# Performance work log

Measured on AMD Instinct MI355X. Metric: run time of the kernel, lower is better.

## Reference

```python
import jax, jax.numpy as jnp
import numpy as np

D_MODEL = 1024
N_HEADS = 16
HEAD_DIM = D_MODEL // N_HEADS


def setup_inputs() -> dict:
    key = jax.random.key(0)
    k_x, k_qkv, k_proj = jax.random.split(key, 3)
    x = jax.random.normal(k_x, (2, 2048, D_MODEL), dtype=jnp.float32)
    # flax nnx.Linear kernels: shape (in_features, out_features), lecun_normal-ish scale
    w_qkv = jax.random.normal(k_qkv, (D_MODEL, 3 * D_MODEL), dtype=jnp.float32) / np.sqrt(D_MODEL)
    w_proj = jax.random.normal(k_proj, (D_MODEL, D_MODEL), dtype=jnp.float32) / np.sqrt(D_MODEL)
    return {"x": x, "w_qkv": w_qkv, "w_proj": w_proj}


def reference(x, w_qkv, w_proj):
    bsz, seq_len, d_model = x.shape
    qkv = x @ w_qkv  # (B, T, 3*D)
    q, k, v = jnp.split(qkv, 3, axis=-1)
    q = q.reshape(bsz, seq_len, N_HEADS, HEAD_DIM)
    k = k.reshape(bsz, seq_len, N_HEADS, HEAD_DIM)
    v = v.reshape(bsz, seq_len, N_HEADS, HEAD_DIM)
    scale = jnp.sqrt(jnp.asarray(HEAD_DIM, dtype=x.dtype))
    attn_logits = jnp.einsum('bthd,bshd->bhts', q / scale, k)  # (B, H, T, T)
    attn_weights = jax.nn.softmax(attn_logits, axis=-1)
    attn_out = jnp.einsum('bhts,bshd->bthd', attn_weights, v)
    attn_out = attn_out.reshape(bsz, seq_len, d_model)
    return attn_out @ w_proj
```

## Files before the change

### kernel.cpp

```cpp
#include <hip/hip_runtime.h>
#include <hip/hip_bf16.h>
#include <cmath>

#define D_MODEL 1024
#define NH 16
#define HD 64
#define BSZ 2
#define SEQ 2048
#define MTOT (BSZ * SEQ)

typedef _Float16 f16x8 __attribute__((ext_vector_type(8)));
typedef __fp16   fp16x2 __attribute__((ext_vector_type(2)));
typedef float    f32x4  __attribute__((ext_vector_type(4)));
typedef float    f32x16 __attribute__((ext_vector_type(16)));
typedef unsigned int uivec2 __attribute__((ext_vector_type(2)));

#define QSCALE 0.18033688011112042f

__device__ __forceinline__ ushort f2h(float x) {
    union { _Float16 h; ushort u; } cv;
    cv.h = (_Float16)x;
    return cv.u;
}
__device__ __forceinline__ uint pkh(float a, float b) {
    union { fp16x2 h; uint u; } cv;
    cv.h = __builtin_amdgcn_cvt_pkrtz(a, b);
    return cv.u;
}
__device__ __forceinline__ float fexp2(float x) {
    float r; asm("v_exp_f32 %0, %1" : "=v"(r) : "v"(x)); return r;
}
__device__ __forceinline__ float fmax3(float a, float b, float c) {
    return fmaxf(fmaxf(a, b), c);
}
__device__ __forceinline__ void gload_lds16(const ushort* g, ushort* l) {
    __builtin_amdgcn_global_load_lds(
        (const __attribute__((address_space(1))) void*)g,
        (__attribute__((address_space(3))) void*)l, 16, 0, 0);
}

__global__ __launch_bounds__(256)
void cast8(const float* __restrict__ in, ushort* __restrict__ out, int n)
{
    const int i = (blockIdx.x * 256 + threadIdx.x) * 8;
    if (i >= n) return;
    float4 a = *(const float4*)(in + i);
    float4 b = *(const float4*)(in + i + 4);
    alignas(16) ushort h8[8];
    h8[0] = f2h(a.x); h8[1] = f2h(a.y); h8[2] = f2h(a.z); h8[3] = f2h(a.w);
    h8[4] = f2h(b.x); h8[5] = f2h(b.y); h8[6] = f2h(b.z); h8[7] = f2h(b.w);
    *(uint4*)(out + i) = *(const uint4*)h8;
}

__global__ __launch_bounds__(256)
void transpose_cast2(const float* __restrict__ A, const float* __restrict__ B,
                     ushort* __restrict__ At, ushort* __restrict__ Bt)
{
    __shared__ float tile[32][33];
    const int z = blockIdx.z;
    const float* in = (z < 3) ? A : B;
    ushort* out     = (z < 3) ? At : Bt;
    const int C     = (z < 3) ? 3 * D_MODEL : D_MODEL;
    const int cb    = (z < 3) ? z * 32 + blockIdx.x : blockIdx.x;
    const int R = D_MODEL;
    const int t  = threadIdx.x;
    const int r0 = blockIdx.y * 32, c0 = cb * 32;
    const int tr = t >> 5, tc = t & 31;
#pragma unroll
    for (int s = 0; s < 4; ++s)
        tile[tr + 8 * s][tc] = in[(size_t)(r0 + tr + 8 * s) * C + c0 + tc];
    __syncthreads();
#pragma unroll
    for (int s = 0; s < 4; ++s)
        out[(size_t)(c0 + tr + 8 * s) * R + r0 + tc] = f2h(tile[tc][tr + 8 * s]);
}

template <int MODE>
__global__ __launch_bounds__(256)
void gemm_mfma(const ushort* __restrict__ A, const ushort* __restrict__ Bt,
               float* __restrict__ outp,
               ushort* __restrict__ Qw, ushort* __restrict__ Kw,
               ushort* __restrict__ Vw, int N)
{
    __shared__ ushort As[2][128 * 32];
    __shared__ ushort Bs[2][128 * 32];

    const int t  = threadIdx.x;
    const int w  = t >> 6;
    const int l  = t & 63;
    const int lr = l & 15;
    const int lg = l >> 4;
    const int wr = w >> 1, wc = w & 1;
    const int m0 = blockIdx.y * 128, n0 = blockIdx.x * 128;

    const ushort* Ab = A  + (size_t)m0 * 1024;
    const ushort* Bb = Bt + (size_t)n0 * 1024;

    f32x4 acc[4][4];
#pragma unroll
    for (int i = 0; i < 4; ++i)
#pragma unroll
        for (int j = 0; j < 4; ++j) acc[i][j] = (f32x4){0.f, 0.f, 0.f, 0.f};

    auto stage = [&](int buf, int k0) {
#pragma unroll
        for (int s = 0; s < 2; ++s) {
            const int c    = s * 64 + l;
            const int row  = w * 32 + (c >> 2);
            const int unit = c & 3;
            gload_lds16(Ab + (size_t)row * 1024 + k0 + unit * 8,
                        &As[buf][(w * 128 + s * 64) * 8]);
            gload_lds16(Bb + (size_t)row * 1024 + k0 + unit * 8,
                        &Bs[buf][(w * 128 + s * 64) * 8]);
        }
    };

    stage(0, 0);
    __syncthreads();

    int cur = 0;
#pragma unroll 4
    for (int kt = 0; kt < 32; ++kt) {
        if (kt + 1 < 32) stage(cur ^ 1, (kt + 1) * 32);

        f16x8 af[4], bf[4];
#pragma unroll
        for (int m = 0; m < 4; ++m)
            af[m] = *(const f16x8*)&As[cur][(wr * 64 + m * 16 + lr) * 32 + lg * 8];
#pragma unroll
        for (int n = 0; n < 4; ++n)
            bf[n] = *(const f16x8*)&Bs[cur][(wc * 64 + n * 16 + lr) * 32 + lg * 8];
#pragma unroll
        for (int m = 0; m < 4; ++m)
#pragma unroll
            for (int n = 0; n < 4; ++n)
                acc[m][n] = __builtin_amdgcn_mfma_f32_16x16x32_f16(
                    af[m], bf[n], acc[m][n], 0, 0, 0);

        __syncthreads();
        cur ^= 1;
    }

    if (MODE == 1) {
#pragma unroll
        for (int mf = 0; mf < 4; ++mf) {
            const int row = m0 + wr * 64 + mf * 16 + lg * 4;
#pragma unroll
            for (int nf = 0; nf < 4; ++nf) {
                const int col = n0 + wc * 64 + nf * 16 + lr;
#pragma unroll
                for (int i = 0; i < 4; ++i)
                    outp[(size_t)(row + i) * N + col] = acc[mf][nf][i];
            }
        }
    } else {
#pragma unroll
        for (int mf = 0; mf < 4; ++mf) {
            const int row = m0 + wr * 64 + mf * 16 + lg * 4;
            const int b   = row >> 11;
            const int tt0 = row & (SEQ - 1);
#pragma unroll
            for (int nf = 0; nf < 4; ++nf) {
                const int col   = n0 + wc * 64 + nf * 16 + lr;
                const int which = col >> 10;
                const int h     = (col >> 6) & 15;
                const int d     = col & 63;
                if (which == 2) {
                    ushort* p = Vw + (((size_t)(b * NH + h) * HD + d) * SEQ) + tt0;
                    alignas(8) ushort e4[4];
#pragma unroll
                    for (int i = 0; i < 4; ++i) e4[i] = f2h(acc[mf][nf][i]);
                    *(uint2*)p = *(const uint2*)e4;
                } else {
                    ushort* dst = (which == 0) ? Qw : Kw;
                    const float sc = (which == 0) ? QSCALE : 1.0f;
#pragma unroll
                    for (int i = 0; i < 4; ++i)
                        dst[((size_t)(b * NH + h) * SEQ + tt0 + i) * HD + d] =
                            f2h(acc[mf][nf][i] * sc);
                }
            }
        }
    }
}

__global__ __launch_bounds__(512, 4)
void attn_mfma7(const ushort* __restrict__ Qw, const ushort* __restrict__ Kw,
                const ushort* __restrict__ Vtg, ushort* __restrict__ AO)
{
    __shared__ ushort KsAll[2][2][64 * 64];
    __shared__ ushort VtAll[2][2][64 * 64];

    const int t    = threadIdx.x;
    const int w    = t >> 6;
    const int l    = t & 63;
    const int q    = l & 31;
    const int hi   = l >> 5;
    const int half = w >> 2;
    const int ww   = w & 3;

    const int bh = blockIdx.y;
    const int q0 = blockIdx.x * 128 + ww * 32;
    const int kbase = half * (SEQ / 2);
    const int NT = (SEQ / 2) / 64;

    const ushort* Qp = Qw  + (size_t)bh * SEQ * HD;
    const ushort* Kp = Kw  + (size_t)bh * SEQ * HD;
    const ushort* Vp = Vtg + (size_t)bh * HD * SEQ;

    ushort (*Ks)[64 * 64] = KsAll[half];
    ushort (*Vt)[64 * 64] = VtAll[half];

    f16x8 qf[4];
#pragma unroll
    for (int kc = 0; kc < 4; ++kc)
        qf[kc] = *(const f16x8*)(Qp + (size_t)(q0 + q) * HD + kc * 16 + hi * 8);

    f32x16 oacc[2];
#pragma unroll
    for (int db = 0; db < 2; ++db)
#pragma unroll
        for (int r = 0; r < 16; ++r) oacc[db][r] = 0.f;
    float m_run = -3.0e38f, l_run = 0.f;

    auto stageK = [&](int buf, int k0) {
#pragma unroll
        for (int s = 0; s < 2; ++s) {
            const int c    = ww * 64 + l + 256 * s;
            const int row  = c >> 3;
            const int unit = (c & 7) ^ (row & 7);
            gload_lds16(Kp + (size_t)(k0 + row) * HD + unit * 8,
                        &Ks[buf][(ww * 64 + 256 * s) * 8]);
        }
    };
    auto stageV = [&](int buf, int k0) {
#pragma unroll
        for (int s = 0; s < 2; ++s) {
            const int c    = ww * 64 + l + 256 * s;
            const int row  = c >> 3;
            const int unit = (c & 7) ^ (row & 7);
            gload_lds16(Vp + (size_t)row * SEQ + k0 + unit * 8,
                        &Vt[buf][(ww * 64 + 256 * s) * 8]);
        }
    };

    stageK(0, kbase);
    stageV(0, kbase);
    __syncthreads();

    int cur = 0;
    for (int kt = 0; kt < NT; ++kt) {
        if (kt + 1 < NT) {
            stageK(cur ^ 1, kbase + (kt + 1) * 64);
            stageV(cur ^ 1, kbase + (kt + 1) * 64);
        }

        f32x16 sacc[2];
        __builtin_amdgcn_s_setprio(1);
#pragma unroll
        for (int kb = 0; kb < 2; ++kb) {
            f32x16 a;
#pragma unroll
            for (int r = 0; r < 16; ++r) a[r] = 0.f;
            const int row = kb * 32 + q;
            const int swz = (row & 7) << 4;
#pragma unroll
            for (int kc = 0; kc < 4; ++kc) {
                f16x8 kf = *(const f16x8*)(
                    (const char*)Ks[cur] + row * 128 + ((kc * 32 + hi * 16) ^ swz));
                a = __builtin_amdgcn_mfma_f32_32x32x16_f16(kf, qf[kc], a, 0, 0, 0);
            }
            sacc[kb] = a;
        }
        __builtin_amdgcn_s_setprio(0);

        float p0 = fmax3(fmaxf(sacc[0][0], sacc[1][0]),
                         fmaxf(sacc[0][1], sacc[1][1]),
                         fmaxf(sacc[0][2], sacc[1][2]));
        float p1 = fmax3(fmaxf(sacc[0][3], sacc[1][3]),
                         fmaxf(sacc[0][4], sacc[1][4]),
                         fmaxf(sacc[0][5], sacc[1][5]));
        float p2 = fmax3(fmaxf(sacc[0][6], sacc[1][6]),
                         fmaxf(sacc[0][7], sacc[1][7]),
                         fmaxf(sacc[0][8], sacc[1][8]));
        float p3 = fmax3(fmaxf(sacc[0][9], sacc[1][9]),
                         fmaxf(sacc[0][10], sacc[1][10]),
                         fmaxf(sacc[0][11], sacc[1][11]));
        float p4 = fmax3(fmaxf(sacc[0][12], sacc[1][12]),
                         fmaxf(sacc[0][13], sacc[1][13]),
                         fmaxf(sacc[0][14], sacc[1][14]));
        float p5 = fmaxf(sacc[0][15], sacc[1][15]);
        float mx = fmaxf(fmax3(p0, p1, p2), fmax3(p3, p4, p5));
        mx = fmaxf(mx, __shfl_xor(mx, 32));

        if (__any(mx > m_run + 8.0f)) {
            const float m_new = fmaxf(m_run, mx);
            const float scale = fexp2(m_run - m_new);
            m_run = m_new;
            l_run *= scale;
#pragma unroll
            for (int db = 0; db < 2; ++db)
#pragma unroll
                for (int r = 0; r < 16; ++r) oacc[db][r] *= scale;
        }

#pragma unroll
        for (int kb = 0; kb < 2; ++kb)
#pragma unroll
            for (int r = 0; r < 16; ++r)
                sacc[kb][r] = fexp2(sacc[kb][r] - m_run);

        float ts[16];
#pragma unroll
        for (int r = 0; r < 16; ++r) ts[r] = sacc[0][r] + sacc[1][r];
#pragma unroll
        for (int s = 8; s > 0; s >>= 1)
#pragma unroll
            for (int r = 0; r < 8; ++r)
                if (r < s) ts[r] += ts[r + s];
        l_run += ts[0] + __shfl_xor(ts[0], 32);

        f16x8 pfrag[4];
#pragma unroll
        for (int kb = 0; kb < 2; ++kb)
#pragma unroll
            for (int lc = 0; lc < 2; ++lc) {
                const int rb = lc * 8;
                uint a = pkh(sacc[kb][rb + 0], sacc[kb][rb + 1]);
                uint b = pkh(sacc[kb][rb + 2], sacc[kb][rb + 3]);
                uint c = pkh(sacc[kb][rb + 4], sacc[kb][rb + 5]);
                uint d = pkh(sacc[kb][rb + 6], sacc[kb][rb + 7]);
                uivec2 r0 = __builtin_amdgcn_permlane32_swap(a, c, false, false);
                uivec2 r1 = __builtin_amdgcn_permlane32_swap(b, d, false, false);
                union { uint u[4]; f16x8 v; } f;
                f.u[0] = r0.x;
                f.u[1] = r1.x;
                f.u[2] = r0.y;
                f.u[3] = r1.y;
                pfrag[kb * 2 + lc] = f.v;
            }

        __builtin_amdgcn_s_setprio(1);
#pragma unroll
        for (int db = 0; db < 2; ++db) {
            const int row = db * 32 + q;
            const int swz = (row & 7) << 4;
#pragma unroll
            for (int kc = 0; kc < 4; ++kc) {
                f16x8 vf = *(const f16x8*)(
                    (const char*)Vt[cur] + row * 128 + ((kc * 32 + hi * 16) ^ swz));
                oacc[db] = __builtin_amdgcn_mfma_f32_32x32x16_f16(
                    vf, pfrag[kc], oacc[db], 0, 0, 0);
            }
        }
        __builtin_amdgcn_s_setprio(0);

        __syncthreads();
        cur ^= 1;
    }

    float* oex = (float*)KsAll;
    float* mex = (float*)VtAll;
    float* lex = mex + 256;

    if (half == 1) {
        mex[ww * 64 + l] = m_run;
        lex[ww * 64 + l] = l_run;
#pragma unroll
        for (int db = 0; db < 2; ++db)
#pragma unroll
            for (int r = 0; r < 16; ++r)
                oex[(((ww * 2 + db) * 16) + r) * 64 + l] = oacc[db][r];
    }
    __syncthreads();
    if (half == 0) {
        const float m2 = mex[ww * 64 + l];
        const float l2 = lex[ww * 64 + l];
        const float mf = fmaxf(m_run, m2);
        float w1 = fexp2(m_run - mf), w2 = fexp2(m2 - mf);
        const float inv = 1.f / (l_run * w1 + l2 * w2);
        w1 *= inv; w2 *= inv;

        const int b = bh >> 4, h = bh & 15;
        ushort* orow = AO + ((size_t)(b * SEQ) + q0 + q) * D_MODEL + h * HD;
#pragma unroll
        for (int db = 0; db < 2; ++db)
#pragma unroll
            for (int g = 0; g < 4; ++g) {
                const int d = db * 32 + g * 8 + hi * 4;
                alignas(8) ushort e4[4];
#pragma unroll
                for (int i = 0; i < 4; ++i) {
                    const float o2 = oex[(((ww * 2 + db) * 16) + g * 4 + i) * 64 + l];
                    e4[i] = f2h(oacc[db][g * 4 + i] * w1 + o2 * w2);
                }
                *(uint2*)(orow + d) = *(const uint2*)e4;
            }
    }
}

extern "C" void kernel_launch(void* const* d_in, const int* in_sizes, int n_in,
                              void* d_out, int out_size, void* d_ws, size_t ws_size,
                              hipStream_t stream)
{
    const float* x      = (const float*)d_in[0];
    const float* w_qkv  = (const float*)d_in[1];
    const float* w_proj = (const float*)d_in[2];
    float* out = (float*)d_out;

    ushort* Xh  = (ushort*)d_ws;
    ushort* WqT = Xh  + (size_t)MTOT * D_MODEL;
    ushort* WpT = WqT + (size_t)3 * D_MODEL * D_MODEL;
    ushort* Qw  = WpT + (size_t)D_MODEL * D_MODEL;
    ushort* Kw  = Qw  + (size_t)MTOT * D_MODEL;
    ushort* Vt  = Kw  + (size_t)MTOT * D_MODEL;
    ushort* AOh = Vt  + (size_t)MTOT * D_MODEL;

    dim3 blk(256);

    cast8<<<dim3(MTOT * D_MODEL / (8 * 256)), blk, 0, stream>>>(x, Xh, MTOT * D_MODEL);
    transpose_cast2<<<dim3(32, 32, 4), blk, 0, stream>>>(w_qkv, w_proj, WqT, WpT);

    gemm_mfma<0><<<dim3(3 * D_MODEL / 128, MTOT / 128), blk, 0, stream>>>(
        Xh, WqT, nullptr, Qw, Kw, Vt, 3 * D_MODEL);

    attn_mfma7<<<dim3(SEQ / 128, BSZ * NH), dim3(512), 0, stream>>>(Qw, Kw, Vt, AOh);

    gemm_mfma<1><<<dim3(D_MODEL / 128, MTOT / 128), blk, 0, stream>>>(
        AOh, WpT, out, nullptr, nullptr, nullptr, D_MODEL);
}
```

Measured before the change: 143.8 us.

## Triple-buffer GEMM LDS staging with explicit vmcnt waits and MFMA priority

Moves the QKV and projection GEMM from double to triple buffering in LDS. Tiles are prefetched two k-steps ahead, and partial s_waitcnt vmcnt waits replace full __syncthreads drains so global loads overlap more compute. It also raises wave priority around the MFMA block. The cost is 50% more LDS per block, which can reduce occupancy, and correctness now depends on hand-counted vmcnt values matching the number of loads issued per stage.

```diff
diff --git a/kernel.cpp b/kernel.cpp
--- a/kernel.cpp
+++ b/kernel.cpp
@@ -82,8 +82,8 @@
                ushort* __restrict__ Qw, ushort* __restrict__ Kw,
                ushort* __restrict__ Vw, int N)
 {
-    __shared__ ushort As[2][128 * 32];
-    __shared__ ushort Bs[2][128 * 32];
+    __shared__ ushort As[3][128 * 32];
+    __shared__ ushort Bs[3][128 * 32];
 
     const int t  = threadIdx.x;
     const int w  = t >> 6;
@@ -102,7 +102,8 @@
 #pragma unroll
         for (int j = 0; j < 4; ++j) acc[i][j] = (f32x4){0.f, 0.f, 0.f, 0.f};
 
-    auto stage = [&](int buf, int k0) {
+    auto stage = [&](int buf, int kt) {
+        const int k0 = kt * 32;
 #pragma unroll
         for (int s = 0; s < 2; ++s) {
             const int c    = s * 64 + l;
@@ -115,31 +116,41 @@
         }
     };
 
-    stage(0, 0);
-    __syncthreads();
-
-    int cur = 0;
-#pragma unroll 4
-    for (int kt = 0; kt < 32; ++kt) {
-        if (kt + 1 < 32) stage(cur ^ 1, (kt + 1) * 32);
+    auto body = [&](int kt, int cb, int vm) {
+        if (kt + 2 < 32) stage((cb + 2) % 3, kt + 2);
+        if (vm == 8)      asm volatile("s_waitcnt vmcnt(8)" ::: "memory");
+        else if (vm == 4) asm volatile("s_waitcnt vmcnt(4)" ::: "memory");
+        else              asm volatile("s_waitcnt vmcnt(0)" ::: "memory");
+        __builtin_amdgcn_s_barrier();
 
         f16x8 af[4], bf[4];
 #pragma unroll
         for (int m = 0; m < 4; ++m)
-            af[m] = *(const f16x8*)&As[cur][(wr * 64 + m * 16 + lr) * 32 + lg * 8];
+            af[m] = *(const f16x8*)&As[cb][(wr * 64 + m * 16 + lr) * 32 + lg * 8];
 #pragma unroll
         for (int n = 0; n < 4; ++n)
-            bf[n] = *(const f16x8*)&Bs[cur][(wc * 64 + n * 16 + lr) * 32 + lg * 8];
+            bf[n] = *(const f16x8*)&Bs[cb][(wc * 64 + n * 16 + lr) * 32 + lg * 8];
+        __builtin_amdgcn_s_setprio(1);
 #pragma unroll
         for (int m = 0; m < 4; ++m)
 #pragma unroll
             for (int n = 0; n < 4; ++n)
                 acc[m][n] = __builtin_amdgcn_mfma_f32_16x16x32_f16(
                     af[m], bf[n], acc[m][n], 0, 0, 0);
-
-        __syncthreads();
-        cur ^= 1;
+        __builtin_amdgcn_s_setprio(0);
+        __builtin_amdgcn_s_barrier();
+    };
+
+    stage(0, 0);
+    stage(1, 1);
+#pragma unroll 1
+    for (int i = 0; i < 10; ++i) {
+        body(i * 3 + 0, 0, 8);
+        body(i * 3 + 1, 1, 8);
+        body(i * 3 + 2, 2, 8);
     }
+    body(30, 0, 4);
+    body(31, 1, 0);
 
     if (MODE == 1) {
 #pragma unroll
```

After: 137.6 us. 1.05x faster.
